# Kernel tuning notes

Hardware: AMD Instinct MI355X
Metric: run time of the kernel (lower is better)

The kernel has to match this reference:

```python
import math
import jax, jax.numpy as jnp
import numpy as np

DIM = 1024
NUM_HEADS = 16
HEAD_DIM = DIM // NUM_HEADS


def rotate_half(x):
    x1, x2 = jnp.split(x, 2, axis=-1)
    return jnp.concatenate((-x2, x1), axis=-1)


def rope_cos_sin(seq_len, head_dim, dtype):
    # angles: (S, D/2); duplicated to (S, D) so it applies to full head_dim
    pos = jnp.arange(seq_len, dtype=dtype)[:, None]
    inv = jnp.exp(jnp.arange(0, head_dim, 2, dtype=dtype) * (-(math.log(10000.0) / head_dim)))
    angles = pos * inv[None, :]
    angles = jnp.concatenate((angles, angles), axis=-1)  # (S, D)
    return jnp.cos(angles), jnp.sin(angles)


def setup_inputs() -> dict:
    key = jax.random.key(0)
    ks = jax.random.split(key, 5)
    B, S, C = 8, 1024, DIM
    scale = 1.0 / math.sqrt(C)
    return {
        "x": jax.random.normal(ks[0], (B, S, C), dtype=jnp.float32),
        "W_qkv": jax.random.normal(ks[1], (C, 3 * C), dtype=jnp.float32) * scale,
        "b_qkv": jax.random.normal(ks[2], (3 * C,), dtype=jnp.float32) * 0.02,
        "W_proj": jax.random.normal(ks[3], (C, C), dtype=jnp.float32) * scale,
        "b_proj": jax.random.normal(ks[4], (C,), dtype=jnp.float32) * 0.02,
    }


def reference(x, W_qkv, b_qkv, W_proj, b_proj):
    B, S, C = x.shape
    H, D = NUM_HEADS, C // NUM_HEADS
    scale = D ** -0.5

    qkv = x @ W_qkv + b_qkv                       # (B, S, 3C)
    qkv = qkv.reshape(B, S, 3, H, D).transpose(2, 0, 3, 1, 4)  # (3, B, H, S, D)
    q, k, v = qkv[0], qkv[1], qkv[2]

    cos, sin = rope_cos_sin(S, D, x.dtype)        # (S, D) each, broadcast over B,H
    q = q * cos + rotate_half(q) * sin
    k = k * cos + rotate_half(k) * sin

    attn = jnp.einsum("bhqd,bhkd->bhqk", q, k) * scale
    attn = jax.nn.softmax(attn, axis=-1)
    out = jnp.einsum("bhqk,bhkd->bhqd", attn, v)  # (B, H, S, D)
    out = out.transpose(0, 2, 1, 3).reshape(B, S, C)
    return out @ W_proj + b_proj
```

## Files before the change

kernel.cpp:

```cpp
#include <hip/hip_runtime.h>
#include <hip/hip_fp16.h>
#include <math.h>


typedef _Float16 half_t;
typedef _Float16 half8 __attribute__((ext_vector_type(8)));
typedef _Float16 half4v __attribute__((ext_vector_type(4)));
typedef float f32x4 __attribute__((ext_vector_type(4)));
typedef float f32x16 __attribute__((ext_vector_type(16)));

#define MFMA16(a, b, c) __builtin_amdgcn_mfma_f32_16x16x32_f16(a, b, c, 0, 0, 0)
#define MFMA32(a, b, c) __builtin_amdgcn_mfma_f32_32x32x16_f16(a, b, c, 0, 0, 0)

__device__ __forceinline__ void gload_lds16(const half_t* g, half_t* lds) {
  __builtin_amdgcn_global_load_lds(
      (const __attribute__((address_space(1))) void*)g,
      (__attribute__((address_space(3))) void*)lds, 16, 0, 0);
}

__device__ __forceinline__ void prep_transpose(const float* __restrict__ in,
                                               half_t* __restrict__ out,
                                               int rows, int cols, int bx,
                                               int by, half_t (*tile)[33]) {
  int c0 = bx * 32, r0 = by * 32;
  int tx = threadIdx.x & 31, g = threadIdx.x >> 5;
#pragma unroll
  for (int i = 0; i < 4; i++) {
    int r = g * 4 + i;
    tile[r][tx] = (half_t)in[(size_t)(r0 + r) * cols + c0 + tx];
  }
  __syncthreads();
#pragma unroll
  for (int i = 0; i < 4; i++) {
    int cc = g * 4 + i;
    out[(size_t)(c0 + cc) * rows + r0 + tx] = tile[tx][cc];
  }
}

__global__ __launch_bounds__(256) void k_prep(
    const float* __restrict__ x, half_t* __restrict__ x16,
    const float* __restrict__ Wqkv, half_t* __restrict__ WqkvT,
    const float* __restrict__ Wproj, half_t* __restrict__ WprojT,
    float2* __restrict__ rope) {
  __shared__ half_t tile[32][33];
  int bid = blockIdx.x;
  if (bid < 8192) {
    int i = bid * 256 + threadIdx.x;
    float4 v = ((const float4*)x)[i];
    half4v h;
    h.x = (half_t)v.x; h.y = (half_t)v.y; h.z = (half_t)v.z; h.w = (half_t)v.w;
    ((half4v*)x16)[i] = h;
  } else if (bid < 11264) {
    int idx = bid - 8192;
    prep_transpose(Wqkv, WqkvT, 1024, 3072, idx % 96, idx / 96, tile);
  } else if (bid < 12288) {
    int idx = bid - 11264;
    prep_transpose(Wproj, WprojT, 1024, 1024, idx & 31, idx >> 5, tile);
  } else {
    int idx = (bid - 12288) * 256 + threadIdx.x;
    int s = idx >> 5, jj = idx & 31;
    float inv = expf(-0.28782313662425572f * (float)jj);
    float ang = (float)s * inv;
    float sn, cs;
    sincosf(ang, &sn, &cs);
    rope[idx] = make_float2(cs, sn);
  }
}

#define GEMM_STAGE(KT, DB)                                                   \
  {                                                                          \
    half_t* As_ = (DB);                                                      \
    half_t* Bs_ = (DB) + 8192;                                               \
    _Pragma("unroll") for (int cc_ = 0; cc_ < 4; cc_++) {                    \
      int lg_ = (w * 4 + cc_) * 64 + lane;                                   \
      int row_ = lg_ >> 3;                                                   \
      int gs_ = (lg_ & 7) ^ (row_ & 7);                                      \
      gload_lds16(A + (size_t)(m0 + row_) * 1024 + (KT) + gs_ * 8,           \
                  As_ + (w * 4 + cc_) * 512);                                \
      gload_lds16(Bt + (size_t)(n0 + row_) * 1024 + (KT) + gs_ * 8,          \
                  Bs_ + (w * 4 + cc_) * 512);                                \
    }                                                                        \
  }

template <int MODE>
__global__ __launch_bounds__(256) void k_gemm(
    const half_t* __restrict__ A, const half_t* __restrict__ Bt,
    const float* __restrict__ bias, const float2* __restrict__ rope,
    half_t* __restrict__ Qo, half_t* __restrict__ Ko, half_t* __restrict__ Vo,
    float* __restrict__ Fo) {
  __shared__ alignas(16) half_t smem[32768];
  const int t = threadIdx.x;
  const int lane = t & 63, w = t >> 6;
  const int c32 = lane & 31, kh = lane >> 5;
  const int m0 = blockIdx.y * 128, n0 = blockIdx.x * 128;
  const int wm = (w >> 1) * 64, wn = (w & 1) * 64;

  f32x16 acc[2][2] = {};

  GEMM_STAGE(0, smem);

  for (int tt = 0; tt < 16; ++tt) {
    half_t* As = smem + (tt & 1) * 16384;
    half_t* Bs = As + 8192;
    if (tt < 15) {
      GEMM_STAGE((tt + 1) * 64, smem + ((tt + 1) & 1) * 16384);
      asm volatile("s_waitcnt vmcnt(8)" ::: "memory");
    } else {
      asm volatile("s_waitcnt vmcnt(0)" ::: "memory");
    }
    __builtin_amdgcn_sched_barrier(0);
    __builtin_amdgcn_s_barrier();
    __builtin_amdgcn_sched_barrier(0);
#pragma unroll
    for (int ks = 0; ks < 4; ks++) {
      half8 af[2], bf[2];
#pragma unroll
      for (int i = 0; i < 2; i++) {
        int mr = wm + i * 32 + c32;
        af[i] = *(const half8*)(As + mr * 64 + (((ks * 2 + kh) ^ (mr & 7)) * 8));
        int nr = wn + i * 32 + c32;
        bf[i] = *(const half8*)(Bs + nr * 64 + (((ks * 2 + kh) ^ (nr & 7)) * 8));
      }
#pragma unroll
      for (int i = 0; i < 2; i++)
#pragma unroll
        for (int j = 0; j < 2; j++) acc[i][j] = MFMA32(af[i], bf[j], acc[i][j]);
    }
    __builtin_amdgcn_sched_barrier(0);
    __builtin_amdgcn_s_barrier();
  }

  if (MODE == 0) {
    const int which = n0 >> 10;
    const int b = m0 >> 10, sbase = m0 & 1023;
    if (which == 2) {
      __syncthreads();
      half_t* T = smem;
#pragma unroll
      for (int i = 0; i < 2; i++)
#pragma unroll
        for (int j = 0; j < 2; j++) {
          int nl = wn + j * 32 + c32;
          float bs = bias[n0 + nl];
#pragma unroll
          for (int a = 0; a < 4; a++) {
            half4v pk;
#pragma unroll
            for (int q = 0; q < 4; q++)
              pk[q] = (half_t)(acc[i][j][a * 4 + q] + bs);
            *(half4v*)(T + nl * 136 + wm + i * 32 + kh * 4 + a * 8) = pk;
          }
        }
      __syncthreads();
#pragma unroll
      for (int u = 0; u < 8; u++) {
        int ci = u * 256 + t;
        int drow = ci >> 4, scol = (ci & 15) * 8;
        half8 val = *(const half8*)(T + drow * 136 + scol);
        int n = n0 + drow;
        int hh = (n >> 6) & 15, d = n & 63;
        *(half8*)(Vo + ((size_t)((b * 16 + hh) * 64 + d)) * 1024 + sbase + scol) = val;
      }
    } else {
      __syncthreads();
      half_t* T = smem;
      const float qsc = (which == 0) ? 0.125f : 1.0f;
#pragma unroll
      for (int i = 0; i < 2; i++)
#pragma unroll
        for (int a = 0; a < 4; a++)
#pragma unroll
          for (int q = 0; q < 4; q++) {
            int ml = wm + i * 32 + a * 8 + kh * 4 + q;
            int s = sbase + ml;
            float2 tr = rope[(s << 5) | c32];
#pragma unroll
            for (int j = 0; j < 2; j++) {
              int nl = wn + j * 32 + c32;
              int n = n0 + nl;
              float v = acc[i][j][a * 4 + q] + bias[n];
              float pr = acc[i][j ^ 1][a * 4 + q] + bias[n ^ 32];
              float rv = (j == 0) ? (v * tr.x - pr * tr.y)
                                  : (v * tr.x + pr * tr.y);
              T[ml * 136 + nl] = (half_t)(rv * qsc);
            }
          }
      __syncthreads();
      half_t* dst = (which == 0) ? Qo : Ko;
#pragma unroll
      for (int u = 0; u < 8; u++) {
        int ci = u * 256 + t;
        int mrow = ci >> 4, ch = ci & 15;
        half8 val = *(const half8*)(T + mrow * 136 + ch * 8);
        int s = sbase + mrow;
        int n = n0 + ch * 8;
        int hh = (n >> 6) & 15, d = n & 63;
        *(half8*)(dst + ((size_t)((b * 16 + hh) * 1024 + s)) * 64 + d) = val;
      }
    }
  } else {
#pragma unroll
    for (int i = 0; i < 2; i++)
#pragma unroll
      for (int a = 0; a < 4; a++)
#pragma unroll
        for (int q = 0; q < 4; q++) {
          int gm = m0 + wm + i * 32 + a * 8 + kh * 4 + q;
#pragma unroll
          for (int j = 0; j < 2; j++) {
            int n = n0 + wn + j * 32 + c32;
            Fo[(size_t)gm * 1024 + n] = acc[i][j][a * 4 + q] + bias[n];
          }
        }
  }
}

__global__ __launch_bounds__(256) void k_attn(const half_t* __restrict__ Qg_,
                                              const half_t* __restrict__ Kg_,
                                              const half_t* __restrict__ Vg_,
                                              half_t* __restrict__ Og) {
  __shared__ alignas(16) half_t Qs[8192];
  __shared__ alignas(16) half_t Ks[4096];
  __shared__ alignas(16) half_t Vs[4096];
  __shared__ alignas(16) half_t Ps[128 * 72];
  __shared__ float ilbuf[128];
  const int t = threadIdx.x, lane = t & 63, w = t >> 6;
  const int quad = lane >> 4, cl = lane & 15;
  const int bh = blockIdx.x, q0 = blockIdx.y * 128;
  const half_t* Qg = Qg_ + (size_t)bh * 65536;
  const half_t* Kg = Kg_ + (size_t)bh * 65536;
  const half_t* Vg = Vg_ + (size_t)bh * 65536;

#pragma unroll
  for (int cc = 0; cc < 4; cc++) {
    int lg = (w * 4 + cc) * 64 + lane;
    int row = lg >> 3;
    int gs = (lg & 7) ^ (row & 7);
    gload_lds16(Qg + (size_t)(q0 + row) * 64 + gs * 8, Qs + (w * 4 + cc) * 512);
  }
  __syncthreads();

  half8 qf[2][2];
#pragma unroll
  for (int ks = 0; ks < 2; ks++)
#pragma unroll
    for (int j = 0; j < 2; j++) {
      int qr = w * 32 + j * 16 + cl;
      qf[ks][j] = *(const half8*)(Qs + qr * 64 + (((ks * 4 + quad) ^ (qr & 7)) * 8));
    }

  f32x4 oacc[2][4] = {};
  float lsum[2] = {0.f, 0.f};

  for (int kt = 0; kt < 1024; kt += 64) {
    __syncthreads();
#pragma unroll
    for (int cc = 0; cc < 2; cc++) {
      int lg = (w * 2 + cc) * 64 + lane;
      int row = lg >> 3;
      int gs = (lg & 7) ^ (row & 7);
      gload_lds16(Kg + (size_t)(kt + row) * 64 + gs * 8, Ks + (w * 2 + cc) * 512);
      gload_lds16(Vg + (size_t)row * 1024 + kt + gs * 8, Vs + (w * 2 + cc) * 512);
    }
    __syncthreads();

    f32x4 sacc[4][2] = {};
#pragma unroll
    for (int ks = 0; ks < 2; ks++) {
      half8 kf[4];
#pragma unroll
      for (int i = 0; i < 4; i++) {
        int kr = i * 16 + cl;
        kf[i] = *(const half8*)(Ks + kr * 64 + (((ks * 4 + quad) ^ (kr & 7)) * 8));
      }
#pragma unroll
      for (int i = 0; i < 4; i++)
#pragma unroll
        for (int j = 0; j < 2; j++)
          sacc[i][j] = MFMA16(kf[i], qf[ks][j], sacc[i][j]);
    }

#pragma unroll
    for (int i = 0; i < 4; i++)
#pragma unroll
      for (int j = 0; j < 2; j++) {
        float p0 = __expf(sacc[i][j][0] - 8.f);
        float p1 = __expf(sacc[i][j][1] - 8.f);
        float p2 = __expf(sacc[i][j][2] - 8.f);
        float p3 = __expf(sacc[i][j][3] - 8.f);
        lsum[j] += (p0 + p1) + (p2 + p3);
        half4v pk;
        pk.x = (half_t)p0; pk.y = (half_t)p1; pk.z = (half_t)p2; pk.w = (half_t)p3;
        *(half4v*)(Ps + (w * 32 + j * 16 + cl) * 72 + i * 16 + quad * 4) = pk;
      }

#pragma unroll
    for (int ks = 0; ks < 2; ks++) {
      half8 pf[2], vf[4];
#pragma unroll
      for (int i = 0; i < 2; i++)
        pf[i] = *(const half8*)(Ps + (w * 32 + i * 16 + cl) * 72 + ks * 32 + quad * 8);
#pragma unroll
      for (int j = 0; j < 4; j++) {
        int dr = j * 16 + cl;
        vf[j] = *(const half8*)(Vs + dr * 64 + (((ks * 4 + quad) ^ (dr & 7)) * 8));
      }
#pragma unroll
      for (int i = 0; i < 2; i++)
#pragma unroll
        for (int j = 0; j < 4; j++) oacc[i][j] = MFMA16(pf[i], vf[j], oacc[i][j]);
    }
  }

#pragma unroll
  for (int j = 0; j < 2; j++) {
    float l = lsum[j];
    l += __shfl_xor(l, 16);
    l += __shfl_xor(l, 32);
    if (quad == 0) ilbuf[w * 32 + j * 16 + cl] = 1.f / l;
  }

  const int b = bh >> 4, hh = bh & 15;
#pragma unroll
  for (int i = 0; i < 2; i++)
#pragma unroll
    for (int r = 0; r < 4; r++) {
      float sc = ilbuf[w * 32 + i * 16 + quad * 4 + r];
      int srow = q0 + w * 32 + i * 16 + quad * 4 + r;
#pragma unroll
      for (int j = 0; j < 4; j++) {
        int d = j * 16 + cl;
        Og[((size_t)(b * 1024 + srow)) * 1024 + hh * 64 + d] =
            (half_t)(oacc[i][j][r] * sc);
      }
    }
}

extern "C" void kernel_launch(void* const* d_in, const int* in_sizes, int n_in,
                              void* d_out, int out_size, void* d_ws,
                              size_t ws_size, hipStream_t stream) {
  (void)in_sizes; (void)n_in; (void)out_size; (void)ws_size;
  const float* x = (const float*)d_in[0];
  const float* Wqkv = (const float*)d_in[1];
  const float* bqkv = (const float*)d_in[2];
  const float* Wproj = (const float*)d_in[3];
  const float* bproj = (const float*)d_in[4];
  float* out = (float*)d_out;

  half_t* ws = (half_t*)d_ws;
  half_t* x16 = ws;
  half_t* WqkvT = ws + 8388608;
  half_t* WprojT = ws + 11534336;
  half_t* Q16 = ws + 12582912;
  half_t* K16 = ws + 20971520;
  half_t* V16 = ws + 29360128;
  float2* rope = (float2*)(ws + 37748736);
  half_t* O16 = x16;

  k_prep<<<12416, 256, 0, stream>>>(x, x16, Wqkv, WqkvT, Wproj, WprojT, rope);
  k_gemm<0><<<dim3(24, 64), 256, 0, stream>>>(x16, WqkvT, bqkv, rope, Q16, K16,
                                              V16, nullptr);
  k_attn<<<dim3(128, 8), 256, 0, stream>>>(Q16, K16, V16, O16);
  k_gemm<1><<<dim3(8, 64), 256, 0, stream>>>(O16, WprojT, bproj, nullptr,
                                             nullptr, nullptr, nullptr, out);
}
```

Measured before the change: 266.3 us.

## Double-buffer K/V tiles in attention kernel and change V-transpose LDS pitch

The attention kernel now prefetches the next K/V tile into a second LDS buffer (reusing the Q staging area after Q fragments are loaded into registers) while computing on the current one. It uses explicit vmcnt waits and raw s_barriers in place of two __syncthreads per iteration, so global-load latency can overlap with the MFMA and softmax work. Separately, the LDS row pitch in the QKV GEMM V-transpose epilogue drops from 136 to 132 halves, which changes the bank-conflict pattern. The manual waitcnt counting and barrier placement add a risk of subtle races, and a 132-half pitch can break 16-byte alignment of the half8 reads.

```diff
diff --git a/kernel.cpp b/kernel.cpp
--- a/kernel.cpp
+++ b/kernel.cpp
@@ -148,7 +148,7 @@
 #pragma unroll
             for (int q = 0; q < 4; q++)
               pk[q] = (half_t)(acc[i][j][a * 4 + q] + bs);
-            *(half4v*)(T + nl * 136 + wm + i * 32 + kh * 4 + a * 8) = pk;
+            *(half4v*)(T + nl * 132 + wm + i * 32 + kh * 4 + a * 8) = pk;
           }
         }
       __syncthreads();
@@ -156,7 +156,7 @@
       for (int u = 0; u < 8; u++) {
         int ci = u * 256 + t;
         int drow = ci >> 4, scol = (ci & 15) * 8;
-        half8 val = *(const half8*)(T + drow * 136 + scol);
+        half8 val = *(const half8*)(T + drow * 132 + scol);
         int n = n0 + drow;
         int hh = (n >> 6) & 15, d = n & 63;
         *(half8*)(Vo + ((size_t)((b * 16 + hh) * 64 + d)) * 1024 + sbase + scol) = val;
@@ -215,15 +215,27 @@
   }
 }
 
+#define ATTN_STAGE_KV(KT, KB)                                                \
+  {                                                                          \
+    _Pragma("unroll") for (int cc_ = 0; cc_ < 2; cc_++) {                    \
+      int lg_ = (w * 2 + cc_) * 64 + lane;                                   \
+      int row_ = lg_ >> 3;                                                   \
+      int gs_ = (lg_ & 7) ^ (row_ & 7);                                      \
+      gload_lds16(Kg + (size_t)((KT) + row_) * 64 + gs_ * 8,                 \
+                  (KB) + (w * 2 + cc_) * 512);                               \
+      gload_lds16(Vg + (size_t)row_ * 1024 + (KT) + gs_ * 8,                 \
+                  (KB) + 4096 + (w * 2 + cc_) * 512);                        \
+    }                                                                        \
+  }
+
 __global__ __launch_bounds__(256) void k_attn(const half_t* __restrict__ Qg_,
                                               const half_t* __restrict__ Kg_,
                                               const half_t* __restrict__ Vg_,
                                               half_t* __restrict__ Og) {
-  __shared__ alignas(16) half_t Qs[8192];
-  __shared__ alignas(16) half_t Ks[4096];
-  __shared__ alignas(16) half_t Vs[4096];
-  __shared__ alignas(16) half_t Ps[128 * 72];
-  __shared__ float ilbuf[128];
+  __shared__ alignas(16) half_t smem[25856];
+  half_t* Qs = smem;
+  half_t* Ps = smem + 16384;
+  float* ilbuf = (float*)(smem + 25600);
   const int t = threadIdx.x, lane = t & 63, w = t >> 6;
   const int quad = lane >> 4, cl = lane & 15;
   const int bh = blockIdx.x, q0 = blockIdx.y * 128;
@@ -238,7 +250,11 @@
     int gs = (lg & 7) ^ (row & 7);
     gload_lds16(Qg + (size_t)(q0 + row) * 64 + gs * 8, Qs + (w * 4 + cc) * 512);
   }
-  __syncthreads();
+  ATTN_STAGE_KV(0, smem + 8192);
+  asm volatile("s_waitcnt vmcnt(4)" ::: "memory");
+  __builtin_amdgcn_sched_barrier(0);
+  __builtin_amdgcn_s_barrier();
+  __builtin_amdgcn_sched_barrier(0);
 
   half8 qf[2][2];
 #pragma unroll
@@ -248,21 +264,23 @@
       int qr = w * 32 + j * 16 + cl;
       qf[ks][j] = *(const half8*)(Qs + qr * 64 + (((ks * 4 + quad) ^ (qr & 7)) * 8));
     }
+  __syncthreads();
 
   f32x4 oacc[2][4] = {};
   float lsum[2] = {0.f, 0.f};
 
-  for (int kt = 0; kt < 1024; kt += 64) {
-    __syncthreads();
-#pragma unroll
-    for (int cc = 0; cc < 2; cc++) {
-      int lg = (w * 2 + cc) * 64 + lane;
-      int row = lg >> 3;
-      int gs = (lg & 7) ^ (row & 7);
-      gload_lds16(Kg + (size_t)(kt + row) * 64 + gs * 8, Ks + (w * 2 + cc) * 512);
-      gload_lds16(Vg + (size_t)row * 1024 + kt + gs * 8, Vs + (w * 2 + cc) * 512);
-    }
-    __syncthreads();
+  for (int tt = 0; tt < 16; ++tt) {
+    const half_t* Kb = smem + ((tt & 1) ? 0 : 8192);
+    const half_t* Vb = Kb + 4096;
+    if (tt < 15) {
+      ATTN_STAGE_KV((tt + 1) * 64, smem + (((tt + 1) & 1) ? 0 : 8192));
+      asm volatile("s_waitcnt vmcnt(4)" ::: "memory");
+    } else {
+      asm volatile("s_waitcnt vmcnt(0)" ::: "memory");
+    }
+    __builtin_amdgcn_sched_barrier(0);
+    __builtin_amdgcn_s_barrier();
+    __builtin_amdgcn_sched_barrier(0);
 
     f32x4 sacc[4][2] = {};
 #pragma unroll
@@ -271,7 +289,7 @@
 #pragma unroll
       for (int i = 0; i < 4; i++) {
         int kr = i * 16 + cl;
-        kf[i] = *(const half8*)(Ks + kr * 64 + (((ks * 4 + quad) ^ (kr & 7)) * 8));
+        kf[i] = *(const half8*)(Kb + kr * 64 + (((ks * 4 + quad) ^ (kr & 7)) * 8));
       }
 #pragma unroll
       for (int i = 0; i < 4; i++)
@@ -303,13 +321,15 @@
 #pragma unroll
       for (int j = 0; j < 4; j++) {
         int dr = j * 16 + cl;
-        vf[j] = *(const half8*)(Vs + dr * 64 + (((ks * 4 + quad) ^ (dr & 7)) * 8));
+        vf[j] = *(const half8*)(Vb + dr * 64 + (((ks * 4 + quad) ^ (dr & 7)) * 8));
       }
 #pragma unroll
       for (int i = 0; i < 2; i++)
 #pragma unroll
         for (int j = 0; j < 4; j++) oacc[i][j] = MFMA16(pf[i], vf[j], oacc[i][j]);
     }
+    __builtin_amdgcn_sched_barrier(0);
+    __builtin_amdgcn_s_barrier();
   }
 
 #pragma unroll
```

After: 251.3 us. -5.6%, faster.
